# Performance work log

Hardware: AMD Instinct MI355X
Metric: run time of the kernel (lower is better)

Reference implementation:

```python
import jax, jax.numpy as jnp
import numpy as np

B, T, V = 64, 32, 50257


def setup_inputs() -> dict:
    key = jax.random.key(0)
    k1, k2, k3 = jax.random.split(key, 3)
    logit_rwc = jax.random.normal(k1, (B, T, V), dtype=jnp.float32)
    cap_rwc_label = jax.random.randint(k2, (B, T), 0, V, dtype=jnp.int32)
    # lengths in [1, T] so every sample has at least one valid position
    cap_len_rwc = jax.random.randint(k3, (B,), 1, T + 1, dtype=jnp.int32)
    return {"logit_rwc": logit_rwc, "cap_rwc_label": cap_rwc_label,
            "cap_len_rwc": cap_len_rwc}


def reference(logit_rwc, cap_rwc_label, cap_len_rwc):
    # model_type == 'OFA': keep label ids > 2
    p = jax.nn.softmax(logit_rwc, axis=2)                      # [B,T,V]
    tmask = (jnp.arange(T)[None, :] < cap_len_rwc[:, None]).astype(p.dtype)
    agg = jnp.einsum('btv,bt->bv', p, tmask)                   # masked sum over valid tokens
    sig = jax.nn.sigmoid(agg)                                  # [B,V]
    lmask = (cap_rwc_label > 2).astype(p.dtype)                # [B,T]
    cnt = lmask.sum(axis=1)                                    # >=1 with overwhelming prob
    prob = jnp.take_along_axis(sig, cap_rwc_label, axis=1)     # [B,T]
    loss_cov = ((-jnp.log(prob)) * lmask).sum(axis=1) / cnt
    prob_sm = jnp.take_along_axis(agg, cap_rwc_label, axis=1)  # [B,T]
    loss_rep = (((1.0 - prob_sm) ** 2) * lmask).sum(axis=1) / cnt
    return loss_cov.mean() + loss_rep.mean()
```

## Files before the change

### kernel.cpp

```cpp
#include <hip/hip_runtime.h>

#define BB 64
#define TT 32
#define VV 50257
#define GRID1 2048

__global__ __launch_bounds__(256) void stream_sumexp(
    const float* __restrict__ logits,
    const int*   __restrict__ labels,
    const int*   __restrict__ lens,
    float*       __restrict__ blk_sum,
    int*         __restrict__ blk_bt,
    float*       __restrict__ numer)
{
    __shared__ int   cum[BB + 1];
    __shared__ float wsum[4];
    const int tid = threadIdx.x;

    if (tid < 64) {
        int inc = lens[tid];
        #pragma unroll
        for (int off = 1; off < 64; off <<= 1) {
            int o = __shfl_up(inc, off);
            if (tid >= off) inc += o;
        }
        cum[tid + 1] = inc;
        if (tid == 0) cum[0] = 0;
    }
    __syncthreads();
    const long long E = (long long)cum[BB] * VV;
    const int e_lo = (int)((E * blockIdx.x) / GRID1);
    const int e_hi = (int)((E * (blockIdx.x + 1)) / GRID1);
    const int r0 = e_lo / VV;
    const int r1 = (e_hi - 1) / VV;

    int c = 0;
    for (int r = r0; r <= r1; ++r, ++c) {
        int lo = 0, hi = BB;
        #pragma unroll
        for (int it = 0; it < 6; ++it) {
            const int mid = (lo + hi) >> 1;
            if (cum[mid] <= r) lo = mid; else hi = mid;
        }
        const int b  = lo;
        const int t  = r - cum[b];
        const int bt = b * TT + t;

        const int rbase = r * VV;
        const int s_loc = (e_lo > rbase ? e_lo : rbase) - rbase;
        const int e_loc = ((e_hi < rbase + VV) ? e_hi : rbase + VV) - rbase;
        const int n = e_loc - s_loc;

        const float* row = logits + (size_t)bt * VV;
        const float* p0  = row + s_loc;

        int head = (int)(((16u - (unsigned)((uintptr_t)p0 & 15u)) & 15u) >> 2);
        if (head > n) head = n;

        float a0 = 0.f, a1 = 0.f, a2 = 0.f, a3 = 0.f;
        for (int i = tid; i < head; i += 256) a0 += __expf(p0[i]);
        const float4* pv = (const float4*)(p0 + head);
        const int nvec = (n - head) >> 2;
        for (int i = tid; i < nvec; i += 256) {
            float4 x = pv[i];
            a0 += __expf(x.x); a1 += __expf(x.y);
            a2 += __expf(x.z); a3 += __expf(x.w);
        }
        for (int k = head + (nvec << 2) + tid; k < n; k += 256) a0 += __expf(p0[k]);

        float acc = (a0 + a1) + (a2 + a3);
        #pragma unroll
        for (int off = 32; off >= 1; off >>= 1) acc += __shfl_xor(acc, off);
        if ((tid & 63) == 0) wsum[tid >> 6] = acc;
        __syncthreads();
        if (tid == 0) {
            blk_sum[blockIdx.x * 2 + c] = (wsum[0] + wsum[1]) + (wsum[2] + wsum[3]);
            blk_bt [blockIdx.x * 2 + c] = bt;
        }

        if (tid < TT) {
            const int l = labels[b * TT + tid];
            if (l >= s_loc && l < e_loc) numer[bt * TT + tid] = __expf(row[l]);
        }
        __syncthreads();
    }
    if (tid == 0 && c < 2) blk_bt[blockIdx.x * 2 + 1] = -1;
}

__global__ __launch_bounds__(256) void loss_reduce(
    const int*   __restrict__ labels,
    const int*   __restrict__ lens,
    const float* __restrict__ blk_sum,
    const int*   __restrict__ blk_bt,
    const float* __restrict__ numer,
    float*       __restrict__ out)
{
    const int b   = blockIdx.x;
    const int tid = threadIdx.x;
    const int len = lens[b];
    const int base = b * TT;

    __shared__ float s_sum[TT];
    __shared__ float s_inv[TT];
    __shared__ float aggp[8][TT];

    if (tid < TT) s_sum[tid] = 0.f;
    __syncthreads();

    for (int i = tid; i < GRID1 * 2; i += 256) {
        const int bt = blk_bt[i];
        if (bt >= base && bt < base + TT) atomicAdd(&s_sum[bt - base], blk_sum[i]);
    }
    __syncthreads();
    if (tid < TT) s_inv[tid] = 1.0f / s_sum[tid];
    __syncthreads();

    const int tg = tid >> 5;
    const int tp = tid & 31;
    float a = 0.f;
    for (int t = tg; t < len; t += 8)
        a += numer[(base + t) * TT + tp] * s_inv[t];
    aggp[tg][tp] = a;
    __syncthreads();

    if (tid < TT) {
        float agg = 0.f;
        #pragma unroll
        for (int q = 0; q < 8; ++q) agg += aggp[q][tid];

        const int l = labels[base + tid];
        float cov = 0.f, rep = 0.f, cnt = 0.f;
        if (l > 2) {
            cov = log1pf(__expf(-agg));
            const float d = 1.0f - agg;
            rep = d * d;
            cnt = 1.0f;
        }
        #pragma unroll
        for (int off = 16; off >= 1; off >>= 1) {
            cov += __shfl_xor(cov, off);
            rep += __shfl_xor(rep, off);
            cnt += __shfl_xor(cnt, off);
        }
        if (tid == 0) atomicAdd(out, (cov + rep) / cnt * (1.0f / BB));
    }
}

extern "C" void kernel_launch(void* const* d_in, const int* in_sizes, int n_in,
                              void* d_out, int out_size, void* d_ws, size_t ws_size,
                              hipStream_t stream) {
    const float* logits = (const float*)d_in[0];
    const int*   labels = (const int*)d_in[1];
    const int*   lens   = (const int*)d_in[2];
    float* out = (float*)d_out;

    float* blk_sum = (float*)d_ws;
    int*   blk_bt  = (int*)((char*)d_ws + GRID1 * 2 * sizeof(float));
    float* numer   = (float*)((char*)d_ws + 2 * GRID1 * 2 * sizeof(float));

    hipMemsetAsync(out, 0, sizeof(float), stream);
    stream_sumexp<<<GRID1, 256, 0, stream>>>(logits, labels, lens, blk_sum, blk_bt, numer);
    loss_reduce<<<BB, 256, 0, stream>>>(labels, lens, blk_sum, blk_bt, numer, out);
}
```

Before: 48.67 us.

## Remove block barriers and numer gather from streaming pass, recompute in reducer

```diff
diff --git a/kernel.cpp b/kernel.cpp
--- a/kernel.cpp
+++ b/kernel.cpp
@@ -7,15 +7,16 @@
 
 __global__ __launch_bounds__(256) void stream_sumexp(
     const float* __restrict__ logits,
-    const int*   __restrict__ labels,
     const int*   __restrict__ lens,
+    int*         __restrict__ blk_bt,
     float*       __restrict__ blk_sum,
-    int*         __restrict__ blk_bt,
-    float*       __restrict__ numer)
+    float*       __restrict__ out)
 {
-    __shared__ int   cum[BB + 1];
-    __shared__ float wsum[4];
+    __shared__ int cum[BB + 1];
     const int tid = threadIdx.x;
+    const int wv  = tid >> 6;
+
+    if (blockIdx.x == 0 && tid == 0) out[0] = 0.f;
 
     if (tid < 64) {
         int inc = lens[tid];
@@ -51,8 +52,7 @@
         const int e_loc = ((e_hi < rbase + VV) ? e_hi : rbase + VV) - rbase;
         const int n = e_loc - s_loc;
 
-        const float* row = logits + (size_t)bt * VV;
-        const float* p0  = row + s_loc;
+        const float* p0 = logits + (size_t)bt * VV + s_loc;
 
         int head = (int)(((16u - (unsigned)((uintptr_t)p0 & 15u)) & 15u) >> 2);
         if (head > n) head = n;
@@ -61,7 +61,16 @@
         for (int i = tid; i < head; i += 256) a0 += __expf(p0[i]);
         const float4* pv = (const float4*)(p0 + head);
         const int nvec = (n - head) >> 2;
-        for (int i = tid; i < nvec; i += 256) {
+        int i = tid;
+        for (; i + 256 < nvec; i += 512) {
+            float4 x = pv[i];
+            float4 y = pv[i + 256];
+            a0 += __expf(x.x) + __expf(y.x);
+            a1 += __expf(x.y) + __expf(y.y);
+            a2 += __expf(x.z) + __expf(y.z);
+            a3 += __expf(x.w) + __expf(y.w);
+        }
+        if (i < nvec) {
             float4 x = pv[i];
             a0 += __expf(x.x); a1 += __expf(x.y);
             a2 += __expf(x.z); a3 += __expf(x.w);
@@ -71,45 +80,40 @@
         float acc = (a0 + a1) + (a2 + a3);
         #pragma unroll
         for (int off = 32; off >= 1; off >>= 1) acc += __shfl_xor(acc, off);
-        if ((tid & 63) == 0) wsum[tid >> 6] = acc;
-        __syncthreads();
-        if (tid == 0) {
-            blk_sum[blockIdx.x * 2 + c] = (wsum[0] + wsum[1]) + (wsum[2] + wsum[3]);
-            blk_bt [blockIdx.x * 2 + c] = bt;
-        }
-
-        if (tid < TT) {
-            const int l = labels[b * TT + tid];
-            if (l >= s_loc && l < e_loc) numer[bt * TT + tid] = __expf(row[l]);
-        }
-        __syncthreads();
+        if ((tid & 63) == 0) blk_sum[((blockIdx.x * 2 + c) << 2) + wv] = acc;
+        if (tid == 0)        blk_bt [blockIdx.x * 2 + c] = bt;
     }
     if (tid == 0 && c < 2) blk_bt[blockIdx.x * 2 + 1] = -1;
 }
 
 __global__ __launch_bounds__(256) void loss_reduce(
+    const float* __restrict__ logits,
     const int*   __restrict__ labels,
     const int*   __restrict__ lens,
+    const int*   __restrict__ blk_bt,
     const float* __restrict__ blk_sum,
-    const int*   __restrict__ blk_bt,
-    const float* __restrict__ numer,
     float*       __restrict__ out)
 {
-    const int b   = blockIdx.x;
-    const int tid = threadIdx.x;
-    const int len = lens[b];
+    const int b    = blockIdx.x;
+    const int tid  = threadIdx.x;
+    const int len  = lens[b];
     const int base = b * TT;
 
     __shared__ float s_sum[TT];
     __shared__ float s_inv[TT];
+    __shared__ int   s_lab[TT];
     __shared__ float aggp[8][TT];
 
-    if (tid < TT) s_sum[tid] = 0.f;
+    if (tid < TT) { s_sum[tid] = 0.f; s_lab[tid] = labels[base + tid]; }
     __syncthreads();
 
+    const float4* bs4 = (const float4*)blk_sum;
     for (int i = tid; i < GRID1 * 2; i += 256) {
         const int bt = blk_bt[i];
-        if (bt >= base && bt < base + TT) atomicAdd(&s_sum[bt - base], blk_sum[i]);
+        if (bt >= base && bt < base + TT) {
+            float4 v = bs4[i];
+            atomicAdd(&s_sum[bt - base], (v.x + v.y) + (v.z + v.w));
+        }
     }
     __syncthreads();
     if (tid < TT) s_inv[tid] = 1.0f / s_sum[tid];
@@ -117,9 +121,10 @@
 
     const int tg = tid >> 5;
     const int tp = tid & 31;
+    const int l  = s_lab[tp];
     float a = 0.f;
     for (int t = tg; t < len; t += 8)
-        a += numer[(base + t) * TT + tp] * s_inv[t];
+        a += __expf(logits[(size_t)(base + t) * VV + l]) * s_inv[t];
     aggp[tg][tp] = a;
     __syncthreads();
 
@@ -128,9 +133,8 @@
         #pragma unroll
         for (int q = 0; q < 8; ++q) agg += aggp[q][tid];
 
-        const int l = labels[base + tid];
         float cov = 0.f, rep = 0.f, cnt = 0.f;
-        if (l > 2) {
+        if (s_lab[tid] > 2) {
             cov = log1pf(__expf(-agg));
             const float d = 1.0f - agg;
             rep = d * d;
@@ -154,11 +158,9 @@
     const int*   lens   = (const int*)d_in[2];
     float* out = (float*)d_out;
 
-    float* blk_sum = (float*)d_ws;
-    int*   blk_bt  = (int*)((char*)d_ws + GRID1 * 2 * sizeof(float));
-    float* numer   = (float*)((char*)d_ws + 2 * GRID1 * 2 * sizeof(float));
+    int*   blk_bt  = (int*)d_ws;
+    float* blk_sum = (float*)((char*)d_ws + GRID1 * 2 * sizeof(int));
 
-    hipMemsetAsync(out, 0, sizeof(float), stream);
-    stream_sumexp<<<GRID1, 256, 0, stream>>>(logits, labels, lens, blk_sum, blk_bt, numer);
-    loss_reduce<<<BB, 256, 0, stream>>>(labels, lens, blk_sum, blk_bt, numer, out);
+    stream_sumexp<<<GRID1, 256, 0, stream>>>(logits, lens, blk_bt, blk_sum, out);
+    loss_reduce<<<BB, 256, 0, stream>>>(logits, labels, lens, blk_bt, blk_sum, out);
 }
```

New measurement: 44.69 us (median of 2 runs). 8.2% less time.
